# Kernel tuning notes

Measured on AMD Instinct MI355X. Metric: run time of the kernel, lower is better.

## Reference

```python
import jax, jax.numpy as jnp
import numpy as np
from jax import lax

B, M, E, H = 16, 64, 256, 256  # batch items, cells per item, n_embedding, n_hidden
S = 4 * M                       # candidate nodes per item (4 per cell)
CLIP = 10.0                     # pointer logit clipping C


def setup_inputs() -> dict:
    key = jax.random.key(0)
    ks = jax.random.split(key, 12)
    sc = 0.05  # keep tanh unsaturated
    return {
        "cell_embed": jax.random.normal(ks[0], (B, S, E), jnp.float32),
        "original_node": jax.random.uniform(ks[1], (B, S, 4), jnp.float32),
        "maze": jnp.zeros((B, 4, 4), jnp.int32),  # unused by the math (torch code builds .tolist() but never uses it)
        "num_cell": M,
        "costs": jax.random.uniform(ks[2], (B, S), jnp.float32),
        "init_w": jax.random.uniform(ks[3], (2 * E,), jnp.float32, -1.0, 1.0),
        "Whc": jax.random.normal(ks[4], (E, E), jnp.float32) * sc,
        "bhc": jax.random.normal(ks[5], (E,), jnp.float32) * sc,
        "Wv": jax.random.normal(ks[6], (2 * E, E), jnp.float32) * sc,
        "bv": jax.random.normal(ks[7], (E,), jnp.float32) * sc,
        "Wq": jax.random.normal(ks[8], (E, H), jnp.float32) * sc,
        "Wk": jax.random.normal(ks[9], (E, H), jnp.float32) * sc,
        "vptr": jax.random.normal(ks[10], (H,), jnp.float32) * sc,
    }


def reference(cell_embed, original_node, maze, num_cell, costs, init_w, Whc, bhc, Wv, bv, Wq, Wk, vptr):
    key = jax.random.key(42)
    bkeys = jax.random.split(key, cell_embed.shape[0])

    def decode_one(emb, node, cost, bkey):
        # emb: [S, E], node: [S, 4], cost: [S]
        h_bar = emb.mean(0) @ Whc + bhc            # h_context_embed(mean)
        k_proj = emb @ Wk                          # [S, H], hoisted out of loop
        q0 = h_bar + init_w @ Wv + bv              # query at step 0

        def step(carry, i):
            query, mask, init_h, st_idx = carry
            # pointer attention: u_j = v^T tanh(Wq q + Wk k_j); logits = C*tanh(u)
            u = jnp.tanh(query @ Wq + k_proj) @ vptr          # [S]
            lg = jnp.where(mask > 0, -1e9, CLIP * jnp.tanh(u))
            idx = jax.random.categorical(jax.random.fold_in(bkey, i), lg)
            logp = jax.nn.log_softmax(lg)[idx]
            # reward: exit point of previous node -> entry point of chosen node, plus internal costs
            ext = jnp.sqrt(jnp.sum((node[idx, :2] - node[st_idx, 2:]) ** 2))
            reward = jnp.where(i > 0, ext + cost[st_idx] + cost[idx], 0.0)
            # mask the whole 4-node cell containing idx, plus idx itself
            mask = lax.dynamic_update_slice(mask, jnp.ones((4,), mask.dtype), (4 * (idx // 4),))
            mask = mask.at[idx].set(1)
            h = emb[idx]                                       # selected node embedding
            init_h = jnp.where(i == 0, h, init_h)
            query = h_bar + jnp.concatenate([init_h, h]) @ Wv + bv
            return (query, mask, init_h, idx), (logp, reward, idx)

        carry0 = (q0, jnp.zeros((emb.shape[0],), jnp.int32),
                  jnp.zeros((emb.shape[1],), emb.dtype), jnp.int32(0))
        _, (logps, rewards, actions) = lax.scan(step, carry0, jnp.arange(num_cell))
        return logps.sum(), rewards.sum(), actions

    lp, rw, act = jax.vmap(decode_one)(cell_embed, original_node, costs, bkeys)
    return lp, rw, act
```

## Files before the change

### kernel.cpp

```cpp
#include <hip/hip_runtime.h>
#include <stdint.h>

#define NB 16
#define NM 64
#define NS 256
#define NE 256
#define NH 256

__device__ __forceinline__ uint32_t rotl32(uint32_t v, int d) { return (v << d) | (v >> (32 - d)); }

__device__ __forceinline__ void threefry(uint32_t k0, uint32_t k1,
                                         uint32_t x0, uint32_t x1,
                                         uint32_t& o0, uint32_t& o1) {
  uint32_t ks2 = k0 ^ k1 ^ 0x1BD11BDAu;
#define TFR(r) { x0 += x1; x1 = rotl32(x1, r); x1 ^= x0; }
  x0 += k0; x1 += k1;
  TFR(13) TFR(15) TFR(26) TFR(6)
  x0 += k1;  x1 += ks2 + 1u;
  TFR(17) TFR(29) TFR(16) TFR(24)
  x0 += ks2; x1 += k0 + 2u;
  TFR(13) TFR(15) TFR(26) TFR(6)
  x0 += k0;  x1 += k1 + 3u;
  TFR(17) TFR(29) TFR(16) TFR(24)
  x0 += k1;  x1 += ks2 + 4u;
  TFR(13) TFR(15) TFR(26) TFR(6)
  x0 += ks2; x1 += k0 + 5u;
#undef TFR
  o0 = x0; o1 = x1;
}

__device__ __forceinline__ float gumbel_from_bits(uint32_t bits) {
  float u = __uint_as_float((bits >> 9) | 0x3f800000u) - 1.0f;
  u = fmaxf(u, 1.17549435e-38f);
  return -logf(-logf(u));
}

__global__ void gumbel_kernel(float* __restrict__ g) {
  const int blk = blockIdx.x;
  const int b = blk >> 6;
  const int i = blk & 63;
  const int s = threadIdx.x;
  uint32_t kb0, kb1, f0, f1, r0, r1;
  threefry(0u, 42u, 0u, (uint32_t)b, kb0, kb1);
  threefry(kb0, kb1, 0u, (uint32_t)i, f0, f1);
  threefry(f0, f1, 0u, (uint32_t)s, r0, r1);
  g[(blk << 8) + s] = gumbel_from_bits(r0 ^ r1);
}

__global__ void prep_kernel(const float* __restrict__ emb,
                            const float* __restrict__ init_w,
                            const float* __restrict__ Whc,
                            const float* __restrict__ bhc,
                            const float* __restrict__ Wv,
                            const float* __restrict__ bv,
                            const float* __restrict__ Wq,
                            float* __restrict__ qbase,
                            float* __restrict__ q0W) {
  const int b = blockIdx.x, t = threadIdx.x;
  __shared__ float mean_s[NE];
  __shared__ float hbpb[NE];
  __shared__ float iwv[NE];
  const float* eb = emb + (size_t)b * NS * NE;
  float acc = 0.f;
  for (int s = 0; s < NS; ++s) acc += eb[s * NE + t];
  mean_s[t] = acc * (1.0f / NS);
  __syncthreads();
  float h = bhc[t];
  for (int j = 0; j < NE; ++j) h = fmaf(mean_s[j], Whc[j * NE + t], h);
  hbpb[t] = h + bv[t];
  float a2 = 0.f;
  for (int j = 0; j < 2 * NE; ++j) a2 = fmaf(init_w[j], Wv[j * NE + t], a2);
  iwv[t] = a2;
  __syncthreads();
  float qb = 0.f, q0 = 0.f;
  for (int e = 0; e < NE; ++e) {
    float w = Wq[e * NH + t];
    qb = fmaf(hbpb[e], w, qb);
    q0 = fmaf(hbpb[e] + iwv[e], w, q0);
  }
  qbase[b * NH + t] = qb;
  q0W[b * NH + t] = q0;
}

__global__ void mm_kernel(const float* __restrict__ A,
                          const float* __restrict__ W,
                          float* __restrict__ C) {
  const int t = threadIdx.x;
  const int hq = (t & 63) * 4;
  const int r0 = (t >> 6) * 4;
  const int rowbase = blockIdx.x * 16;
  float acc[4][4] = {};
  #pragma unroll 2
  for (int e = 0; e < NE; ++e) {
    float4 w = *(const float4*)(W + e * NH + hq);
    #pragma unroll
    for (int r = 0; r < 4; ++r) {
      float a = A[(size_t)(rowbase + r0 + r) * NE + e];
      acc[r][0] = fmaf(a, w.x, acc[r][0]);
      acc[r][1] = fmaf(a, w.y, acc[r][1]);
      acc[r][2] = fmaf(a, w.z, acc[r][2]);
      acc[r][3] = fmaf(a, w.w, acc[r][3]);
    }
  }
  #pragma unroll
  for (int r = 0; r < 4; ++r)
    *(float4*)(C + (size_t)(rowbase + r0 + r) * NH + hq) =
        make_float4(acc[r][0], acc[r][1], acc[r][2], acc[r][3]);
}

__global__ void expqb_kernel(float* __restrict__ QB) {
  const size_t i = (size_t)blockIdx.x * 1024 + threadIdx.x;
  QB[i] = __expf(2.0f * QB[i]);
}

#define PIDX(h) (((h) >> 5) * 36 + ((h) & 31))

__global__ __launch_bounds__(1024, 4) void decode_kernel(
    const float* __restrict__ emb,
    const float* __restrict__ node,
    const float* __restrict__ costs,
    const float* __restrict__ Wv,
    const float* __restrict__ Wq,
    const float* __restrict__ vptr,
    const float* __restrict__ g_g,
    const float* __restrict__ kp_g,
    const float* __restrict__ EQB_g,
    const float* __restrict__ qbase_g,
    const float* __restrict__ q0W_g,
    float* __restrict__ out) {
  const int b = blockIdx.x;
  const int tid = threadIdx.x;
  const int hc = tid & 7;
  const int pr = tid >> 3;
  const int s0 = pr * 2, s1 = s0 + 1;

  __shared__ float qWp[8 * 36];
  __shared__ float vpp[8 * 36];
  __shared__ float lg_s[NS];
  __shared__ float val_s[NS];
  __shared__ float red_v[4];
  __shared__ int   red_i[4];
  __shared__ float red_ml[4];
  __shared__ float red_e[4];
  __shared__ int   idx_hist[NM];
  __shared__ float er[NE];
  __shared__ float Ts[NE];

  float4 ek0[8], ek1[8];
  {
    const float4* p0 = (const float4*)(kp_g + ((size_t)b * NS + s0) * NH + hc * 32);
    const float4* p1 = (const float4*)(kp_g + ((size_t)b * NS + s1) * NH + hc * 32);
    #pragma unroll
    for (int j = 0; j < 8; ++j) {
      float4 a = p0[j], c = p1[j];
      ek0[j] = make_float4(__expf(2.f * a.x), __expf(2.f * a.y), __expf(2.f * a.z), __expf(2.f * a.w));
      ek1[j] = make_float4(__expf(2.f * c.x), __expf(2.f * c.y), __expf(2.f * c.z), __expf(2.f * c.w));
    }
  }
  float Vsum = 0.f;
  {
    const float4* vv = (const float4*)(vptr + hc * 32);
    #pragma unroll
    for (int j = 0; j < 8; ++j) { float4 v = vv[j]; Vsum += (v.x + v.y) + (v.z + v.w); }
  }
  if (tid < NH) {
    vpp[PIDX(tid)] = -2.0f * vptr[tid];
    qWp[PIDX(tid)] = __expf(2.0f * q0W_g[b * NH + tid]);
  }
  float e2qb = (tid < NH) ? __expf(2.0f * qbase_g[b * NH + tid]) : 0.f;

  int m = 0, pend = 0;
  float logp = 0.f;
  const float* gb = g_g + (size_t)b * NM * NS;

  __syncthreads();

  for (int i = 0; i < NM; ++i) {
    if (pend) {
      pend = 0;
      if (hc == 0) {
        lg_s[s0] = -1e9f; val_s[s0] = -1e9f;
        lg_s[s1] = -1e9f; val_s[s1] = -1e9f;
      }
    } else if (!m) {
      float2 g01 = make_float2(0.f, 0.f);
      if (hc == 0) g01 = *(const float2*)(gb + i * NS + s0);
      const float4* q4 = (const float4*)(qWp + hc * 36);
      const float4* v4 = (const float4*)(vpp + hc * 36);
      float a0 = 0.f, a1 = 0.f;
      #pragma unroll
      for (int jj = 0; jj < 4; ++jj) {
        float4 qa = q4[2 * jj], qb = q4[2 * jj + 1];
        float4 va = v4[2 * jj], vb = v4[2 * jj + 1];
        {
          float4 ka = ek0[2 * jj], kb = ek0[2 * jj + 1];
          float z1 = fmaf(qa.x, ka.x, 1.f), z2 = fmaf(qa.y, ka.y, 1.f);
          float z3 = fmaf(qa.z, ka.z, 1.f), z4 = fmaf(qa.w, ka.w, 1.f);
          float z5 = fmaf(qb.x, kb.x, 1.f), z6 = fmaf(qb.y, kb.y, 1.f);
          float z7 = fmaf(qb.z, kb.z, 1.f), z8 = fmaf(qb.w, kb.w, 1.f);
          float p12 = z1 * z2, p34 = z3 * z4, p56 = z5 * z6, p78 = z7 * z8;
          float p1234 = p12 * p34, p5678 = p56 * p78;
          float r = __builtin_amdgcn_rcpf(p1234 * p5678);
          float t12 = fmaf(va.y, z1, va.x * z2);
          float t34 = fmaf(va.w, z3, va.z * z4);
          float t56 = fmaf(vb.y, z5, vb.x * z6);
          float t78 = fmaf(vb.w, z7, vb.z * z8);
          float T14 = fmaf(t34, p12, t12 * p34);
          float T58 = fmaf(t78, p56, t56 * p78);
          a0 = fmaf(T14 * p5678, r, a0);
          a0 = fmaf(T58 * p1234, r, a0);
        }
        {
          float4 ka = ek1[2 * jj], kb = ek1[2 * jj + 1];
          float z1 = fmaf(qa.x, ka.x, 1.f), z2 = fmaf(qa.y, ka.y, 1.f);
          float z3 = fmaf(qa.z, ka.z, 1.f), z4 = fmaf(qa.w, ka.w, 1.f);
          float z5 = fmaf(qb.x, kb.x, 1.f), z6 = fmaf(qb.y, kb.y, 1.f);
          float z7 = fmaf(qb.z, kb.z, 1.f), z8 = fmaf(qb.w, kb.w, 1.f);
          float p12 = z1 * z2, p34 = z3 * z4, p56 = z5 * z6, p78 = z7 * z8;
          float p1234 = p12 * p34, p5678 = p56 * p78;
          float r = __builtin_amdgcn_rcpf(p1234 * p5678);
          float t12 = fmaf(va.y, z1, va.x * z2);
          float t34 = fmaf(va.w, z3, va.z * z4);
          float t56 = fmaf(vb.y, z5, vb.x * z6);
          float t78 = fmaf(vb.w, z7, vb.z * z8);
          float T14 = fmaf(t34, p12, t12 * p34);
          float T58 = fmaf(t78, p56, t56 * p78);
          a1 = fmaf(T14 * p5678, r, a1);
          a1 = fmaf(T58 * p1234, r, a1);
        }
      }
      float u0 = Vsum + a0;
      float u1 = Vsum + a1;
      u0 += __shfl_xor(u0, 1); u0 += __shfl_xor(u0, 2); u0 += __shfl_xor(u0, 4);
      u1 += __shfl_xor(u1, 1); u1 += __shfl_xor(u1, 2); u1 += __shfl_xor(u1, 4);
      if (hc == 0) {
        float ex0 = __expf(2.f * u0);
        float ex1 = __expf(2.f * u1);
        float lg0 = fmaf(-20.f, __builtin_amdgcn_rcpf(ex0 + 1.f), 10.f);
        float lg1 = fmaf(-20.f, __builtin_amdgcn_rcpf(ex1 + 1.f), 10.f);
        lg_s[s0] = lg0; val_s[s0] = lg0 + g01.x;
        lg_s[s1] = lg1; val_s[s1] = lg1 + g01.y;
      }
    }
    __syncthreads();

    if (tid < NS) {
      float lgl = lg_s[tid];
      float v = val_s[tid]; int vi = tid; float ml = lgl;
      #pragma unroll
      for (int off = 1; off < 64; off <<= 1) {
        float ov = __shfl_xor(v, off);
        int   oi = __shfl_xor(vi, off);
        bool take = (ov > v) || (ov == v && oi < vi);
        v  = take ? ov : v;
        vi = take ? oi : vi;
        ml = fmaxf(ml, __shfl_xor(ml, off));
      }
      float e = __expf(lgl - ml);
      #pragma unroll
      for (int off = 1; off < 64; off <<= 1) e += __shfl_xor(e, off);
      if ((tid & 63) == 0) {
        red_v[tid >> 6] = v; red_i[tid >> 6] = vi;
        red_ml[tid >> 6] = ml; red_e[tid >> 6] = e;
      }
    }
    __syncthreads();

    float bvv = red_v[0]; int bii = red_i[0];
    #pragma unroll
    for (int w = 1; w < 4; ++w) {
      bool take = (red_v[w] > bvv) || (red_v[w] == bvv && red_i[w] < bii);
      bvv = take ? red_v[w] : bvv;
      bii = take ? red_i[w] : bii;
    }
    const int idx = bii;

    if (tid == 0) {
      float ml = fmaxf(fmaxf(red_ml[0], red_ml[1]), fmaxf(red_ml[2], red_ml[3]));
      float sum = 0.f;
      #pragma unroll
      for (int w = 0; w < 4; ++w) sum += red_e[w] * __expf(red_ml[w] - ml);
      logp += lg_s[idx] - (ml + logf(sum));
      idx_hist[i] = idx;
      out[2 * NB + b * NM + i] = (float)idx;
    }

    if (!m && (pr >> 1) == (idx >> 2)) { m = 1; pend = 1; }

    if (i == 0) {
      if (tid < NE) er[tid] = emb[((size_t)b * NS + idx) * NE + tid];
      __syncthreads();
      if (tid < NE) {
        float tv = 0.f;
        #pragma unroll 4
        for (int j = 0; j < NE; ++j) tv = fmaf(er[j], Wv[j * NE + tid], tv);
        Ts[tid] = tv;
      }
      __syncthreads();
      if (tid < NE) {
        float qi = 0.f;
        #pragma unroll 4
        for (int e2 = 0; e2 < NE; ++e2) qi = fmaf(Ts[e2], Wq[e2 * NH + tid], qi);
        e2qb *= __expf(2.0f * qi);
      }
    }

    if (tid < NH) qWp[PIDX(tid)] = e2qb * EQB_g[((size_t)b * NS + idx) * NH + tid];
    __syncthreads();
  }

  if (tid == 0) out[b] = logp;

  if (tid < 64) {
    float term = 0.f;
    if (tid > 0) {
      int id = idx_hist[tid];
      int pv = idx_hist[tid - 1];
      float dx = node[((size_t)b * NS + id) * 4 + 0] - node[((size_t)b * NS + pv) * 4 + 2];
      float dy = node[((size_t)b * NS + id) * 4 + 1] - node[((size_t)b * NS + pv) * 4 + 3];
      term = sqrtf(dx * dx + dy * dy) + costs[(size_t)b * NS + pv] + costs[(size_t)b * NS + id];
    }
    #pragma unroll
    for (int off = 1; off < 64; off <<= 1) term += __shfl_xor(term, off);
    if (tid == 0) out[NB + b] = term;
  }
}

extern "C" void kernel_launch(void* const* d_in, const int* in_sizes, int n_in,
                              void* d_out, int out_size, void* d_ws, size_t ws_size,
                              hipStream_t stream) {
  const float* emb    = (const float*)d_in[0];
  const float* node   = (const float*)d_in[1];
  const float* costs  = (const float*)d_in[4];
  const float* init_w = (const float*)d_in[5];
  const float* Whc    = (const float*)d_in[6];
  const float* bhc    = (const float*)d_in[7];
  const float* Wv     = (const float*)d_in[8];
  const float* bv     = (const float*)d_in[9];
  const float* Wq     = (const float*)d_in[10];
  const float* Wk     = (const float*)d_in[11];
  const float* vptr   = (const float*)d_in[12];
  float* out = (float*)d_out;

  float* ws    = (float*)d_ws;
  float* g     = ws;
  float* kp    = g + NB * NM * NS;
  float* QB    = kp + (size_t)NB * NS * NH;
  float* tmpB  = QB + (size_t)NB * NS * NH;
  float* qbase = tmpB + (size_t)NB * NS * NE;
  float* q0W   = qbase + NB * NH;

  gumbel_kernel<<<NB * NM, 256, 0, stream>>>(g);
  prep_kernel<<<NB, NE, 0, stream>>>(emb, init_w, Whc, bhc, Wv, bv, Wq, qbase, q0W);
  mm_kernel<<<NB * NS / 16, 256, 0, stream>>>(emb, Wk, kp);
  mm_kernel<<<NB * NS / 16, 256, 0, stream>>>(emb, Wv + NE * NE, tmpB);
  mm_kernel<<<NB * NS / 16, 256, 0, stream>>>(tmpB, Wq, QB);
  expqb_kernel<<<(NB * NS * NH) / 1024, 1024, 0, stream>>>(QB);
  decode_kernel<<<NB, 1024, 0, stream>>>(emb, node, costs, Wv, Wq, vptr,
                                         g, kp, QB, qbase, q0W, out);
}
```

Baseline: 398.8 us.

## Fuse per-step argmax and softmax reductions into all waves, drop a barrier

The per-step reduction is restructured. Every wave now reduces its own pairs of logits in registers (max, sum-exp, argmax carrying the chosen logit) and writes one partial per wave. The old path staged values to shared memory and reduced them in 4 waves behind an extra barrier. The logsumexp is no longer finished serially by thread 0 each step; per-step partials are stored and finalised once after the loop. This removes one __syncthreads and a serial tail from each of the 64 sequential steps, at the cost of 8x redundant shuffle work across the hc lanes.

```diff
diff --git a/kernel.cpp b/kernel.cpp
--- a/kernel.cpp
+++ b/kernel.cpp
@@ -133,15 +133,14 @@
   const int hc = tid & 7;
   const int pr = tid >> 3;
   const int s0 = pr * 2, s1 = s0 + 1;
+  const int wid = tid >> 6;
+  const int lane = tid & 63;
 
   __shared__ float qWp[8 * 36];
   __shared__ float vpp[8 * 36];
-  __shared__ float lg_s[NS];
-  __shared__ float val_s[NS];
-  __shared__ float red_v[4];
-  __shared__ int   red_i[4];
-  __shared__ float red_ml[4];
-  __shared__ float red_e[4];
+  __shared__ float4 part4[16];
+  __shared__ float2 mle[NM][17];
+  __shared__ float blg_hist[NM];
   __shared__ int   idx_hist[NM];
   __shared__ float er[NE];
   __shared__ float Ts[NE];
@@ -169,22 +168,15 @@
   }
   float e2qb = (tid < NH) ? __expf(2.0f * qbase_g[b * NH + tid]) : 0.f;
 
-  int m = 0, pend = 0;
-  float logp = 0.f;
+  int m = 0;
   const float* gb = g_g + (size_t)b * NM * NS;
 
   __syncthreads();
 
   for (int i = 0; i < NM; ++i) {
-    if (pend) {
-      pend = 0;
-      if (hc == 0) {
-        lg_s[s0] = -1e9f; val_s[s0] = -1e9f;
-        lg_s[s1] = -1e9f; val_s[s1] = -1e9f;
-      }
-    } else if (!m) {
-      float2 g01 = make_float2(0.f, 0.f);
-      if (hc == 0) g01 = *(const float2*)(gb + i * NS + s0);
+    float lg0, lg1, val0, val1;
+    if (!m) {
+      float2 g01 = *(const float2*)(gb + i * NS + s0);
       const float4* q4 = (const float4*)(qWp + hc * 36);
       const float4* v4 = (const float4*)(vpp + hc * 36);
       float a0 = 0.f, a1 = 0.f;
@@ -233,59 +225,57 @@
       float u1 = Vsum + a1;
       u0 += __shfl_xor(u0, 1); u0 += __shfl_xor(u0, 2); u0 += __shfl_xor(u0, 4);
       u1 += __shfl_xor(u1, 1); u1 += __shfl_xor(u1, 2); u1 += __shfl_xor(u1, 4);
-      if (hc == 0) {
-        float ex0 = __expf(2.f * u0);
-        float ex1 = __expf(2.f * u1);
-        float lg0 = fmaf(-20.f, __builtin_amdgcn_rcpf(ex0 + 1.f), 10.f);
-        float lg1 = fmaf(-20.f, __builtin_amdgcn_rcpf(ex1 + 1.f), 10.f);
-        lg_s[s0] = lg0; val_s[s0] = lg0 + g01.x;
-        lg_s[s1] = lg1; val_s[s1] = lg1 + g01.y;
-      }
+      float ex0 = __expf(2.f * u0);
+      float ex1 = __expf(2.f * u1);
+      lg0 = fmaf(-20.f, __builtin_amdgcn_rcpf(ex0 + 1.f), 10.f);
+      lg1 = fmaf(-20.f, __builtin_amdgcn_rcpf(ex1 + 1.f), 10.f);
+      val0 = lg0 + g01.x;
+      val1 = lg1 + g01.y;
+    } else {
+      lg0 = -1e9f; lg1 = -1e9f; val0 = -1e9f; val1 = -1e9f;
+    }
+    float ml = fmaxf(lg0, lg1);
+    #pragma unroll
+    for (int off = 1; off < 64; off <<= 1) ml = fmaxf(ml, __shfl_xor(ml, off));
+    float e = (__expf(lg0 - ml) + __expf(lg1 - ml)) * 0.125f;
+    #pragma unroll
+    for (int off = 1; off < 64; off <<= 1) e += __shfl_xor(e, off);
+    bool t1 = val1 > val0;
+    float v = t1 ? val1 : val0;
+    int vi = t1 ? s1 : s0;
+    float lgw = t1 ? lg1 : lg0;
+    #pragma unroll
+    for (int off = 1; off < 64; off <<= 1) {
+      float ov = __shfl_xor(v, off);
+      int   oi = __shfl_xor(vi, off);
+      float ol = __shfl_xor(lgw, off);
+      bool take = (ov > v) || (ov == v && oi < vi);
+      v   = take ? ov : v;
+      vi  = take ? oi : vi;
+      lgw = take ? ol : lgw;
+    }
+    if (lane == 0) {
+      part4[wid] = make_float4(v, __int_as_float(vi), lgw, 0.f);
+      mle[i][wid] = make_float2(ml, e);
     }
     __syncthreads();
 
-    if (tid < NS) {
-      float lgl = lg_s[tid];
-      float v = val_s[tid]; int vi = tid; float ml = lgl;
-      #pragma unroll
-      for (int off = 1; off < 64; off <<= 1) {
-        float ov = __shfl_xor(v, off);
-        int   oi = __shfl_xor(vi, off);
-        bool take = (ov > v) || (ov == v && oi < vi);
-        v  = take ? ov : v;
-        vi = take ? oi : vi;
-        ml = fmaxf(ml, __shfl_xor(ml, off));
-      }
-      float e = __expf(lgl - ml);
-      #pragma unroll
-      for (int off = 1; off < 64; off <<= 1) e += __shfl_xor(e, off);
-      if ((tid & 63) == 0) {
-        red_v[tid >> 6] = v; red_i[tid >> 6] = vi;
-        red_ml[tid >> 6] = ml; red_e[tid >> 6] = e;
-      }
-    }
-    __syncthreads();
-
-    float bvv = red_v[0]; int bii = red_i[0];
-    #pragma unroll
-    for (int w = 1; w < 4; ++w) {
-      bool take = (red_v[w] > bvv) || (red_v[w] == bvv && red_i[w] < bii);
-      bvv = take ? red_v[w] : bvv;
-      bii = take ? red_i[w] : bii;
-    }
-    const int idx = bii;
-
-    if (tid == 0) {
-      float ml = fmaxf(fmaxf(red_ml[0], red_ml[1]), fmaxf(red_ml[2], red_ml[3]));
-      float sum = 0.f;
-      #pragma unroll
-      for (int w = 0; w < 4; ++w) sum += red_e[w] * __expf(red_ml[w] - ml);
-      logp += lg_s[idx] - (ml + logf(sum));
-      idx_hist[i] = idx;
-      out[2 * NB + b * NM + i] = (float)idx;
-    }
-
-    if (!m && (pr >> 1) == (idx >> 2)) { m = 1; pend = 1; }
+    float4 p = part4[lane & 15];
+    float cv = p.x; int ci = __float_as_int(p.y); float cl = p.z;
+    #pragma unroll
+    for (int off = 1; off < 16; off <<= 1) {
+      float ov = __shfl_xor(cv, off);
+      int   oi = __shfl_xor(ci, off);
+      float ol = __shfl_xor(cl, off);
+      bool take = (ov > cv) || (ov == cv && oi < ci);
+      cv = take ? ov : cv;
+      ci = take ? oi : ci;
+      cl = take ? ol : cl;
+    }
+    const int idx = ci;
+    if (tid == 0) { idx_hist[i] = idx; blg_hist[i] = cl; }
+
+    if (!m && (pr >> 1) == (idx >> 2)) m = 1;
 
     if (i == 0) {
       if (tid < NE) er[tid] = emb[((size_t)b * NS + idx) * NE + tid];
@@ -309,20 +299,33 @@
     __syncthreads();
   }
 
-  if (tid == 0) out[b] = logp;
-
-  if (tid < 64) {
+  if (wid == 0) {
+    float mlg = -3.0e38f;
+    #pragma unroll 4
+    for (int w = 0; w < 16; ++w) mlg = fmaxf(mlg, mle[lane][w].x);
+    float sum = 0.f;
+    #pragma unroll 4
+    for (int w = 0; w < 16; ++w) {
+      float2 me = mle[lane][w];
+      sum += me.y * __expf(me.x - mlg);
+    }
+    float term = blg_hist[lane] - (mlg + logf(sum));
+    #pragma unroll
+    for (int off = 1; off < 64; off <<= 1) term += __shfl_xor(term, off);
+    if (lane == 0) out[b] = term;
+    out[2 * NB + b * NM + lane] = (float)idx_hist[lane];
+  } else if (wid == 1) {
     float term = 0.f;
-    if (tid > 0) {
-      int id = idx_hist[tid];
-      int pv = idx_hist[tid - 1];
+    if (lane > 0) {
+      int id = idx_hist[lane];
+      int pv = idx_hist[lane - 1];
       float dx = node[((size_t)b * NS + id) * 4 + 0] - node[((size_t)b * NS + pv) * 4 + 2];
       float dy = node[((size_t)b * NS + id) * 4 + 1] - node[((size_t)b * NS + pv) * 4 + 3];
       term = sqrtf(dx * dx + dy * dy) + costs[(size_t)b * NS + pv] + costs[(size_t)b * NS + id];
     }
     #pragma unroll
     for (int off = 1; off < 64; off <<= 1) term += __shfl_xor(term, off);
-    if (tid == 0) out[NB + b] = term;
+    if (lane == 0) out[NB + b] = term;
   }
 }
 
```

Measured after the change: 378.8 us. 1.05x faster.
